# Kernel optimization log

Hardware: AMD Instinct MI355X
Metric: run time of the kernel (lower is better)

The kernel has to match this reference:

```python
import jax, jax.numpy as jnp
import numpy as np

B, S, D = 8, 2048, 512

def setup_inputs() -> dict:
    key = jax.random.key(0)
    k1, k2, k3 = jax.random.split(key, 3)
    context = jax.random.normal(k1, (B, S, D), dtype=jnp.float32)
    # nn.Linear default init ~ U(-1/sqrt(D), 1/sqrt(D)); scale keeps softmax sane
    bound = 1.0 / np.sqrt(D)
    W_in = jax.random.uniform(k2, (D, D), dtype=jnp.float32, minval=-bound, maxval=bound)
    W_out = jax.random.uniform(k3, (D, D), dtype=jnp.float32, minval=-bound, maxval=bound)
    return {"context": context, "W_in": W_in, "W_out": W_out}

def reference(context, W_in, W_out):
    # linear_in: x @ W_in.T (torch Linear convention)
    c = jnp.einsum('bsd,ed->bse', context, W_in)            # [B,S,D]
    scores = jnp.einsum('bsd,btd->bst', c, c)               # [B,S,S], no 1/sqrt(d) scale
    attn = jax.nn.softmax(scores, axis=-1)                  # [B,S,S]
    ctx = jnp.einsum('bst,btd->bsd', attn, c)               # [B,S,D]
    out = jnp.einsum('bsd,ed->bse', jnp.tanh(ctx), W_out)   # linear_out
    return out, attn
```

## Files before the change

kernel.cpp:

```cpp
#include <hip/hip_runtime.h>
#include <cstdint>
#include <cstddef>

#define Bc 8
#define Sc 2048
#define Dc 512

typedef float f32x4 __attribute__((ext_vector_type(4)));
typedef __bf16 bf16x8 __attribute__((ext_vector_type(8)));
typedef __bf16 bf16x4 __attribute__((ext_vector_type(4)));

__device__ __forceinline__ void gload_lds16(const void* g, void* l) {
    __builtin_amdgcn_global_load_lds((const __attribute__((address_space(1))) void*)g,
                                     (__attribute__((address_space(3))) void*)l, 16, 0, 0);
}

__device__ __forceinline__ f32x4 mfma16x16x32(bf16x8 a, bf16x8 b, f32x4 c) {
    return __builtin_amdgcn_mfma_f32_16x16x32_bf16(a, b, c, 0, 0, 0);
}

__global__ void k_convert_w(const float* __restrict__ wi, const float* __restrict__ wo,
                            __bf16* __restrict__ wib, __bf16* __restrict__ wob) {
    int i = blockIdx.x * 256 + threadIdx.x;
    wib[i] = (__bf16)wi[i];
    wob[i] = (__bf16)wo[i];
}

template <bool STATS>
__global__ __launch_bounds__(256) void k_gemm_bf16(
        const __bf16* __restrict__ A, const __bf16* __restrict__ Bt,
        float* __restrict__ C, float2* __restrict__ stats,
        int lda, int ldb, int ldc, int K,
        size_t aOffZ, size_t bOffZ, size_t cOffZ)
{
    __shared__ alignas(16) __bf16 smem[2 * 128 * 64];
    __bf16* As = smem;
    __bf16* Bs = smem + 128 * 64;
    const int tid  = threadIdx.x;
    const int wave = tid >> 6, lane = tid & 63;
    const int waveM = wave >> 1, waveN = wave & 1;
    int row0, col0, bz;
    if constexpr (STATS) {
        const int bid = blockIdx.x;
        bz   = bid & 7;
        col0 = ((bid >> 3) & 15) * 128;
        row0 = (bid >> 7) * 128;
    } else {
        bz = blockIdx.z; row0 = blockIdx.y * 128; col0 = blockIdx.x * 128;
    }
    A  += (size_t)bz * aOffZ;
    Bt += (size_t)bz * bOffZ;
    C  += (size_t)bz * cOffZ;

    f32x4 acc[4][4] = {};

    for (int k0 = 0; k0 < K; k0 += 64) {
        #pragma unroll
        for (int i = 0; i < 4; ++i) {
            int flat = i * 2048 + wave * 512 + lane * 8;
            int r  = flat >> 6;
            int cc = (flat >> 3) & 7;
            int gc = (cc ^ (r & 7)) << 3;
            gload_lds16(A  + (size_t)(row0 + r) * lda + k0 + gc, As + i * 2048 + wave * 512);
            gload_lds16(Bt + (size_t)(col0 + r) * ldb + k0 + gc, Bs + i * 2048 + wave * 512);
        }
        __syncthreads();
        #pragma unroll
        for (int ks = 0; ks < 2; ++ks) {
            const int kc = ks * 4 + (lane >> 4);
            bf16x8 av[4], bv[4];
            #pragma unroll
            for (int mi = 0; mi < 4; ++mi) {
                int r = waveM * 64 + mi * 16 + (lane & 15);
                av[mi] = *(const bf16x8*)&As[r * 64 + ((kc ^ (r & 7)) << 3)];
            }
            #pragma unroll
            for (int ni = 0; ni < 4; ++ni) {
                int r = waveN * 64 + ni * 16 + (lane & 15);
                bv[ni] = *(const bf16x8*)&Bs[r * 64 + ((kc ^ (r & 7)) << 3)];
            }
            #pragma unroll
            for (int mi = 0; mi < 4; ++mi)
                #pragma unroll
                for (int ni = 0; ni < 4; ++ni)
                    acc[mi][ni] = mfma16x16x32(av[mi], bv[ni], acc[mi][ni]);
        }
        __syncthreads();
    }

    const int rb = (lane >> 4) << 2;
    const int cb = lane & 15;
    #pragma unroll
    for (int mi = 0; mi < 4; ++mi)
        #pragma unroll
        for (int ni = 0; ni < 4; ++ni) {
            int gr = row0 + waveM * 64 + mi * 16 + rb;
            int gc = col0 + waveN * 64 + ni * 16 + cb;
            #pragma unroll
            for (int rr = 0; rr < 4; ++rr)
                C[(size_t)(gr + rr) * ldc + gc] = acc[mi][ni][rr];
        }

    if constexpr (STATS) {
        float2* sm = (float2*)smem;
        #pragma unroll
        for (int mi = 0; mi < 4; ++mi)
            #pragma unroll
            for (int rr = 0; rr < 4; ++rr) {
                float mx = fmaxf(fmaxf(acc[mi][0][rr], acc[mi][1][rr]),
                                 fmaxf(acc[mi][2][rr], acc[mi][3][rr]));
                #pragma unroll
                for (int off = 1; off < 16; off <<= 1) mx = fmaxf(mx, __shfl_xor(mx, off));
                float zs = 0.f;
                #pragma unroll
                for (int ni = 0; ni < 4; ++ni) zs += __expf(acc[mi][ni][rr] - mx);
                #pragma unroll
                for (int off = 1; off < 16; off <<= 1) zs += __shfl_xor(zs, off);
                if ((lane & 15) == 0)
                    sm[waveN * 128 + waveM * 64 + mi * 16 + rb + rr] = make_float2(mx, zs);
            }
        __syncthreads();
        if (tid < 128) {
            float2 a2 = sm[tid], b2 = sm[128 + tid];
            float M = fmaxf(a2.x, b2.x);
            float Z = a2.y * __expf(a2.x - M) + b2.y * __expf(b2.x - M);
            stats[((size_t)bz * Sc + row0 + tid) * 16 + (col0 >> 7)] = make_float2(M, Z);
        }
    }
}

__global__ __launch_bounds__(256) void k_stat_combine(const float2* __restrict__ stats,
                                                      float2* __restrict__ rowstat) {
    int r = blockIdx.x * 256 + threadIdx.x;
    float2 s[16];
    #pragma unroll
    for (int i = 0; i < 16; ++i) s[i] = stats[(size_t)r * 16 + i];
    float M = s[0].x;
    #pragma unroll
    for (int i = 1; i < 16; ++i) M = fmaxf(M, s[i].x);
    float Z = 0.f;
    #pragma unroll
    for (int i = 0; i < 16; ++i) Z += s[i].y * __expf(s[i].x - M);
    rowstat[r] = make_float2(M, 1.f / Z);
}

__global__ __launch_bounds__(512) void k_pv_fused(
        float* __restrict__ attn,
        const __bf16* __restrict__ cT,
        const float2* __restrict__ rowstat,
        __bf16* __restrict__ ctx)
{
    __shared__ alignas(16) __bf16 As[64 * 64];
    const int tid  = threadIdx.x;
    const int wave = tid >> 6, lane = tid & 63;
    const int b    = blockIdx.x & 7;
    const int row0 = (blockIdx.x >> 3) * 64;
    float* sc = attn + (size_t)b * Sc * Sc;
    const __bf16* Bt = cT + (size_t)b * Dc * Sc;

    const int ar = tid >> 3;
    const int ac = (tid & 7) * 8;
    const float2 st = rowstat[b * Sc + row0 + ar];
    const float m_row = st.x, zinv = st.y;
    const int a_addr = ar * 64 + ((((ac >> 3)) ^ (ar & 7)) << 3);
    float* srow = sc + (size_t)(row0 + ar) * Sc + ac;

    const __bf16* bbase[4];
    #pragma unroll
    for (int ni = 0; ni < 4; ++ni)
        bbase[ni] = Bt + (size_t)(wave * 64 + ni * 16 + (lane & 15)) * Sc + (lane >> 4) * 8;

    f32x4 acc[4][4] = {};

    const int NT = Sc / 64;

    f32x4 sn0 = *(const f32x4*)&srow[0];
    f32x4 sn1 = *(const f32x4*)&srow[4];
    {
        f32x4 p0, p1;
        #pragma unroll
        for (int j = 0; j < 4; ++j) {
            p0[j] = __expf(sn0[j] - m_row) * zinv;
            p1[j] = __expf(sn1[j] - m_row) * zinv;
        }
        bf16x8 pb;
        #pragma unroll
        for (int j = 0; j < 4; ++j) { pb[j] = (__bf16)p0[j]; pb[4 + j] = (__bf16)p1[j]; }
        *(bf16x8*)&As[a_addr] = pb;
        *(f32x4*)&srow[0] = p0;
        *(f32x4*)&srow[4] = p1;
    }
    asm volatile("s_waitcnt lgkmcnt(0)" ::: "memory");
    __builtin_amdgcn_s_barrier();
    sn0 = *(const f32x4*)&srow[64];
    sn1 = *(const f32x4*)&srow[68];

    for (int t = 0; t < NT; ++t) {
        bf16x8 av[4][2];
        #pragma unroll
        for (int ks = 0; ks < 2; ++ks) {
            const int kc = ks * 4 + (lane >> 4);
            #pragma unroll
            for (int mi = 0; mi < 4; ++mi) {
                int r = mi * 16 + (lane & 15);
                av[mi][ks] = *(const bf16x8*)&As[r * 64 + ((kc ^ (r & 7)) << 3)];
            }
        }
        __builtin_amdgcn_s_barrier();
        if (t + 1 < NT) {
            f32x4 p0, p1;
            #pragma unroll
            for (int j = 0; j < 4; ++j) {
                p0[j] = __expf(sn0[j] - m_row) * zinv;
                p1[j] = __expf(sn1[j] - m_row) * zinv;
            }
            bf16x8 pb;
            #pragma unroll
            for (int j = 0; j < 4; ++j) { pb[j] = (__bf16)p0[j]; pb[4 + j] = (__bf16)p1[j]; }
            *(bf16x8*)&As[a_addr] = pb;
            *(f32x4*)&srow[(t + 1) * 64]     = p0;
            *(f32x4*)&srow[(t + 1) * 64 + 4] = p1;
            if (t + 2 < NT) {
                sn0 = *(const f32x4*)&srow[(t + 2) * 64];
                sn1 = *(const f32x4*)&srow[(t + 2) * 64 + 4];
            }
        }
        const int kt = t * 64;
        bf16x8 bv[2][4];
        #pragma unroll
        for (int ks = 0; ks < 2; ++ks)
            #pragma unroll
            for (int ni = 0; ni < 4; ++ni)
                bv[ks][ni] = *(const bf16x8*)(bbase[ni] + kt + ks * 32);
        #pragma unroll
        for (int ks = 0; ks < 2; ++ks)
            #pragma unroll
            for (int mi = 0; mi < 4; ++mi)
                #pragma unroll
                for (int ni = 0; ni < 4; ++ni)
                    acc[mi][ni] = mfma16x16x32(av[mi][ks], bv[ks][ni], acc[mi][ni]);
        asm volatile("s_waitcnt lgkmcnt(0)" ::: "memory");
        __builtin_amdgcn_s_barrier();
    }

    const int rb = (lane >> 4) << 2;
    const int cb = lane & 15;
    #pragma unroll
    for (int mi = 0; mi < 4; ++mi)
        #pragma unroll
        for (int ni = 0; ni < 4; ++ni) {
            int gr = row0 + mi * 16 + rb;
            int gc = wave * 64 + ni * 16 + cb;
            #pragma unroll
            for (int rr = 0; rr < 4; ++rr)
                ctx[(size_t)(b * Sc + gr + rr) * Dc + gc] = (__bf16)tanhf(acc[mi][ni][rr]);
        }
}

__global__ __launch_bounds__(256) void k_cproj(
        const float* __restrict__ A, const __bf16* __restrict__ Bt,
        __bf16* __restrict__ Cb, __bf16* __restrict__ CTb)
{
    __shared__ alignas(16) char smem[49152];
    float*  Asf = (float*)smem;
    __bf16* Bs  = (__bf16*)(smem + 32768);
    const int tid  = threadIdx.x;
    const int wave = tid >> 6, lane = tid & 63;
    const int waveM = wave >> 1, waveN = wave & 1;
    const int row0 = blockIdx.y * 128;
    const int col0 = blockIdx.x * 128;

    f32x4 acc[4][4] = {};

    for (int k0 = 0; k0 < Dc; k0 += 64) {
        #pragma unroll
        for (int i = 0; i < 8; ++i) {
            int flat = i * 1024 + wave * 256 + lane * 4;
            int r  = flat >> 6;
            int cc = (flat >> 2) & 15;
            int gc = (cc ^ (r & 15)) << 2;
            gload_lds16(A + (size_t)(row0 + r) * Dc + k0 + gc, Asf + i * 1024 + wave * 256);
        }
        #pragma unroll
        for (int i = 0; i < 4; ++i) {
            int flat = i * 2048 + wave * 512 + lane * 8;
            int r  = flat >> 6;
            int cc = (flat >> 3) & 7;
            int gc = (cc ^ (r & 7)) << 3;
            gload_lds16(Bt + (size_t)(col0 + r) * Dc + k0 + gc, Bs + i * 2048 + wave * 512);
        }
        __syncthreads();
        #pragma unroll
        for (int ks = 0; ks < 2; ++ks) {
            const int kc8 = ks * 4 + (lane >> 4);
            const int kc4 = kc8 << 1;
            bf16x8 av[4], bv[4];
            #pragma unroll
            for (int mi = 0; mi < 4; ++mi) {
                int r  = waveM * 64 + mi * 16 + (lane & 15);
                int r4 = r & 15;
                f32x4 lo = *(const f32x4*)&Asf[r * 64 + (((kc4    ) ^ r4) << 2)];
                f32x4 hi = *(const f32x4*)&Asf[r * 64 + (((kc4 + 1) ^ r4) << 2)];
                bf16x8 a;
                a[0] = (__bf16)lo[0]; a[1] = (__bf16)lo[1]; a[2] = (__bf16)lo[2]; a[3] = (__bf16)lo[3];
                a[4] = (__bf16)hi[0]; a[5] = (__bf16)hi[1]; a[6] = (__bf16)hi[2]; a[7] = (__bf16)hi[3];
                av[mi] = a;
            }
            #pragma unroll
            for (int ni = 0; ni < 4; ++ni) {
                int r = waveN * 64 + ni * 16 + (lane & 15);
                bv[ni] = *(const bf16x8*)&Bs[r * 64 + ((kc8 ^ (r & 7)) << 3)];
            }
            #pragma unroll
            for (int mi = 0; mi < 4; ++mi)
                #pragma unroll
                for (int ni = 0; ni < 4; ++ni)
                    acc[mi][ni] = mfma16x16x32(av[mi], bv[ni], acc[mi][ni]);
        }
        __syncthreads();
    }

    const int rb = (lane >> 4) << 2;
    const int cb = lane & 15;
    __bf16* T = (__bf16*)smem;
    #pragma unroll
    for (int mi = 0; mi < 4; ++mi)
        #pragma unroll
        for (int ni = 0; ni < 4; ++ni) {
            int lr = waveM * 64 + mi * 16 + rb;
            int lc = waveN * 64 + ni * 16 + cb;
            #pragma unroll
            for (int rr = 0; rr < 4; ++rr) {
                __bf16 h = (__bf16)acc[mi][ni][rr];
                Cb[(size_t)(row0 + lr + rr) * Dc + col0 + lc] = h;
                T[lc * 136 + lr + rr] = h;
            }
        }
    __syncthreads();
    const int bb = row0 >> 11;
    const int s0 = row0 & 2047;
    #pragma unroll
    for (int i = 0; i < 8; ++i) {
        int n  = i * 16 + (tid >> 4);
        int mo = (tid & 15) * 8;
        bf16x8 v = *(const bf16x8*)&T[n * 136 + mo];
        *(bf16x8*)&CTb[(size_t)bb * Dc * Sc + (size_t)(col0 + n) * Sc + s0 + mo] = v;
    }
}

extern "C" void kernel_launch(void* const* d_in, const int* in_sizes, int n_in,
                              void* d_out, int out_size, void* d_ws, size_t ws_size,
                              hipStream_t stream)
{
    (void)in_sizes; (void)n_in; (void)out_size; (void)ws_size;
    const float* context = (const float*)d_in[0];
    const float* W_in    = (const float*)d_in[1];
    const float* W_out   = (const float*)d_in[2];
    float* out  = (float*)d_out;
    float* attn = out + (size_t)Bc * Sc * Dc;

    char* ws = (char*)d_ws;
    __bf16* c_bf    = (__bf16*)ws;
    __bf16* cT_bf   = (__bf16*)(ws + 16777216);
    __bf16* wi_bf   = (__bf16*)(ws + 33554432);
    __bf16* wo_bf   = (__bf16*)(ws + 34078720);
    float2* stats   = (float2*)(ws + 34603008);
    float2* rowstat = (float2*)(ws + 36700160);

    k_convert_w<<<dim3(Dc * Dc / 256), 256, 0, stream>>>(W_in, W_out, wi_bf, wo_bf);

    k_cproj<<<dim3(Dc / 128, (Bc * Sc) / 128), 256, 0, stream>>>(context, wi_bf, c_bf, cT_bf);

    k_gemm_bf16<true><<<dim3(Bc * 16 * 16), 256, 0, stream>>>(
        c_bf, c_bf, attn, stats, Dc, Dc, Sc, Dc,
        (size_t)Sc * Dc, (size_t)Sc * Dc, (size_t)Sc * Sc);

    k_stat_combine<<<dim3(Bc * Sc / 256), 256, 0, stream>>>(stats, rowstat);

    k_pv_fused<<<dim3((Sc / 64) * Bc), 512, 0, stream>>>(attn, cT_bf, rowstat, c_bf);

    k_gemm_bf16<false><<<dim3(Dc / 128, (Bc * Sc) / 128, 1), 256, 0, stream>>>(
        c_bf, wo_bf, out, nullptr, Dc, Dc, Dc, Dc, 0, 0, 0);
}
```

Baseline: 213.3 us.

## Double-buffer B-operand register loads and defer attn writeback in PV kernel

In the fused softmax-normalise plus PV matmul kernel, the B operand (cT) tiles now go into two alternating register buffers, so the next tile's global loads are issued before the current tile's MFMAs. The loop is unrolled by two to swap the buffers. The normalised probability writeback to attn is delayed by one iteration so the store overlaps compute. Sched barriers pin instruction order around the LDS waits, and launch bounds request two blocks per CU, which raises register pressure from the extra buffer and risks spills.

```diff
diff --git a/kernel.cpp b/kernel.cpp
--- a/kernel.cpp
+++ b/kernel.cpp
@@ -144,7 +144,7 @@
     rowstat[r] = make_float2(M, 1.f / Z);
 }
 
-__global__ __launch_bounds__(512) void k_pv_fused(
+__global__ __launch_bounds__(512, 2) void k_pv_fused(
         float* __restrict__ attn,
         const __bf16* __restrict__ cT,
         const float2* __restrict__ rowstat,
@@ -162,7 +162,7 @@
     const int ac = (tid & 7) * 8;
     const float2 st = rowstat[b * Sc + row0 + ar];
     const float m_row = st.x, zinv = st.y;
-    const int a_addr = ar * 64 + ((((ac >> 3)) ^ (ar & 7)) << 3);
+    const int a_addr = ar * 64 + (((ac >> 3) ^ (ar & 7)) << 3);
     float* srow = sc + (size_t)(row0 + ar) * Sc + ac;
 
     const __bf16* bbase[4];
@@ -171,31 +171,39 @@
         bbase[ni] = Bt + (size_t)(wave * 64 + ni * 16 + (lane & 15)) * Sc + (lane >> 4) * 8;
 
     f32x4 acc[4][4] = {};
-
     const int NT = Sc / 64;
 
-    f32x4 sn0 = *(const f32x4*)&srow[0];
-    f32x4 sn1 = *(const f32x4*)&srow[4];
+    bf16x8 bvA[2][4], bvB[2][4];
+    auto loadB = [&](bf16x8 (&bv)[2][4], int kt) {
+        #pragma unroll
+        for (int ks = 0; ks < 2; ++ks)
+            #pragma unroll
+            for (int ni = 0; ni < 4; ++ni)
+                bv[ks][ni] = *(const bf16x8*)(bbase[ni] + kt + ks * 32);
+    };
+
+    f32x4 pca, pcb;
     {
-        f32x4 p0, p1;
+        f32x4 sa = *(const f32x4*)&srow[0];
+        f32x4 sb = *(const f32x4*)&srow[4];
         #pragma unroll
         for (int j = 0; j < 4; ++j) {
-            p0[j] = __expf(sn0[j] - m_row) * zinv;
-            p1[j] = __expf(sn1[j] - m_row) * zinv;
-        }
-        bf16x8 pb;
-        #pragma unroll
-        for (int j = 0; j < 4; ++j) { pb[j] = (__bf16)p0[j]; pb[4 + j] = (__bf16)p1[j]; }
-        *(bf16x8*)&As[a_addr] = pb;
-        *(f32x4*)&srow[0] = p0;
-        *(f32x4*)&srow[4] = p1;
-    }
+            pca[j] = __expf(sa[j] - m_row) * zinv;
+            pcb[j] = __expf(sb[j] - m_row) * zinv;
+        }
+        bf16x8 pb8;
+        #pragma unroll
+        for (int j = 0; j < 4; ++j) { pb8[j] = (__bf16)pca[j]; pb8[4 + j] = (__bf16)pcb[j]; }
+        *(bf16x8*)&As[a_addr] = pb8;
+    }
+    loadB(bvA, 0);
+    f32x4 sna = *(const f32x4*)&srow[64];
+    f32x4 snb = *(const f32x4*)&srow[68];
     asm volatile("s_waitcnt lgkmcnt(0)" ::: "memory");
+    __builtin_amdgcn_sched_barrier(0);
     __builtin_amdgcn_s_barrier();
-    sn0 = *(const f32x4*)&srow[64];
-    sn1 = *(const f32x4*)&srow[68];
-
-    for (int t = 0; t < NT; ++t) {
+
+    auto body = [&](bf16x8 (&cur)[2][4], bf16x8 (&nxt)[2][4], int t) {
         bf16x8 av[4][2];
         #pragma unroll
         for (int ks = 0; ks < 2; ++ks) {
@@ -206,41 +214,49 @@
                 av[mi][ks] = *(const bf16x8*)&As[r * 64 + ((kc ^ (r & 7)) << 3)];
             }
         }
+        asm volatile("s_waitcnt lgkmcnt(0)" ::: "memory");
+        __builtin_amdgcn_sched_barrier(0);
         __builtin_amdgcn_s_barrier();
         if (t + 1 < NT) {
-            f32x4 p0, p1;
+            f32x4 pna, pnb;
             #pragma unroll
             for (int j = 0; j < 4; ++j) {
-                p0[j] = __expf(sn0[j] - m_row) * zinv;
-                p1[j] = __expf(sn1[j] - m_row) * zinv;
-            }
-            bf16x8 pb;
-            #pragma unroll
-            for (int j = 0; j < 4; ++j) { pb[j] = (__bf16)p0[j]; pb[4 + j] = (__bf16)p1[j]; }
-            *(bf16x8*)&As[a_addr] = pb;
-            *(f32x4*)&srow[(t + 1) * 64]     = p0;
-            *(f32x4*)&srow[(t + 1) * 64 + 4] = p1;
+                pna[j] = __expf(sna[j] - m_row) * zinv;
+                pnb[j] = __expf(snb[j] - m_row) * zinv;
+            }
+            bf16x8 pb8;
+            #pragma unroll
+            for (int j = 0; j < 4; ++j) { pb8[j] = (__bf16)pna[j]; pb8[4 + j] = (__bf16)pnb[j]; }
+            *(bf16x8*)&As[a_addr] = pb8;
+            loadB(nxt, (t + 1) * 64);
+            *(f32x4*)&srow[t * 64]     = pca;
+            *(f32x4*)&srow[t * 64 + 4] = pcb;
             if (t + 2 < NT) {
-                sn0 = *(const f32x4*)&srow[(t + 2) * 64];
-                sn1 = *(const f32x4*)&srow[(t + 2) * 64 + 4];
-            }
-        }
-        const int kt = t * 64;
-        bf16x8 bv[2][4];
+                sna = *(const f32x4*)&srow[(t + 2) * 64];
+                snb = *(const f32x4*)&srow[(t + 2) * 64 + 4];
+            }
+            pca = pna; pcb = pnb;
+        } else {
+            *(f32x4*)&srow[t * 64]     = pca;
+            *(f32x4*)&srow[t * 64 + 4] = pcb;
+        }
         #pragma unroll
         for (int ks = 0; ks < 2; ++ks)
             #pragma unroll
-            for (int ni = 0; ni < 4; ++ni)
-                bv[ks][ni] = *(const bf16x8*)(bbase[ni] + kt + ks * 32);
-        #pragma unroll
-        for (int ks = 0; ks < 2; ++ks)
-            #pragma unroll
             for (int mi = 0; mi < 4; ++mi)
                 #pragma unroll
                 for (int ni = 0; ni < 4; ++ni)
-                    acc[mi][ni] = mfma16x16x32(av[mi][ks], bv[ks][ni], acc[mi][ni]);
-        asm volatile("s_waitcnt lgkmcnt(0)" ::: "memory");
-        __builtin_amdgcn_s_barrier();
+                    acc[mi][ni] = mfma16x16x32(av[mi][ks], cur[ks][ni], acc[mi][ni]);
+        if (t + 1 < NT) {
+            asm volatile("s_waitcnt lgkmcnt(0)" ::: "memory");
+            __builtin_amdgcn_sched_barrier(0);
+            __builtin_amdgcn_s_barrier();
+        }
+    };
+
+    for (int t = 0; t < NT; t += 2) {
+        body(bvA, bvB, t);
+        body(bvB, bvA, t + 1);
     }
 
     const int rb = (lane >> 4) << 2;
```

After: 216.1 us. About the same (+1.3%).
